# Kernel optimization log

Hardware: AMD Instinct MI355X
Metric: run time of the kernel (lower is better)

Reference implementation:

```python
import jax, jax.numpy as jnp
import numpy as np

T, D = 8192, 1024      # num flattened tokens, hidden_dim
E, K = 8, 2            # n_experts, num_experts_per_tok


def setup_inputs() -> dict:
    key = jax.random.key(0)
    k1, k2, k3, k4, k5 = jax.random.split(key, 5)
    x = jax.random.normal(k1, (T, D), dtype=jnp.float32)
    flat_expert_indices = jax.random.randint(k2, (T * K,), 0, E, dtype=jnp.int32)
    flat_expert_weights = jax.random.uniform(k3, (T * K,), dtype=jnp.float32)
    # Expert params: fc1/fc2 are bias-free Linears, stored torch-style [out, in]
    W1 = jax.random.normal(k4, (E, D, D), dtype=jnp.float32) * (1.0 / np.sqrt(D))
    W2 = jax.random.normal(k5, (E, D, D), dtype=jnp.float32) * (1.0 / np.sqrt(D))
    return {"x": x, "flat_expert_indices": flat_expert_indices,
            "flat_expert_weights": flat_expert_weights, "W1": W1, "W2": W2}


def reference(x, flat_expert_indices, flat_expert_weights, W1, W2):
    # DummyExpert: relu(relu(x @ W1.T) @ W2.T), per expert (torch Linear = x @ W.T)
    # Dense dispatch: compute every expert on every token, then gather the
    # top-k expert outputs per token and combine with routing weights.
    h = jax.nn.relu(jnp.einsum('td,eod->eto', x, W1))   # [E, T, D]
    y = jax.nn.relu(jnp.einsum('eto,epo->etp', h, W2))  # [E, T, D]
    idx = flat_expert_indices.reshape(T, K)             # [T, K]
    w = flat_expert_weights.reshape(T, K)               # [T, K]
    yt = jnp.transpose(y, (1, 0, 2))                    # [T, E, D]
    sel = jnp.take_along_axis(yt, idx[:, :, None].astype(jnp.int32), axis=1)  # [T, K, D]
    return jnp.sum(sel * w[:, :, None], axis=1)         # [T, D]
```

## Files before the change

kernel.cpp:

```cpp
#include <hip/hip_runtime.h>

typedef unsigned short u16;
typedef unsigned int   u32;
typedef unsigned long long u64;
typedef __attribute__((ext_vector_type(8))) short short8;
typedef __attribute__((ext_vector_type(4))) float f32x4;

#define T_TOK 8192
#define DIM   1024
#define NEXP  8
#define NPAIR (T_TOK * 2)
#define MAXTILES 136

__device__ __forceinline__ u16 f2bf(float f) {
  u32 u = __builtin_bit_cast(u32, f);
  u32 r = (u + 0x7fffu + ((u >> 16) & 1u)) >> 16;
  return (u16)r;
}
__device__ __forceinline__ float bf2f(u16 b) {
  return __builtin_bit_cast(float, ((u32)b) << 16);
}

__device__ __forceinline__ void gl_lds16(const u16* g, u16* l) {
  __builtin_amdgcn_global_load_lds(
      (const __attribute__((address_space(1))) u32*)g,
      (__attribute__((address_space(3))) u32*)l,
      16, 0, 0);
}

__global__ void prep_k(const float* __restrict__ x, const float* __restrict__ W1,
                       const float* __restrict__ W2,
                       u16* __restrict__ xb, u16* __restrict__ w1b, u16* __restrict__ w2b,
                       const int* __restrict__ idx,
                       int* __restrict__ counts, int* __restrict__ offsets,
                       int* __restrict__ bucket, int* __restrict__ pos,
                       int* __restrict__ tlist, int* __restrict__ ntiles) {
  __shared__ int lc[16][NEXP];
  __shared__ int lo[16][NEXP];

  if (blockIdx.x != 0) {
    const int g = ((int)(blockIdx.x - 1) * 1024 + (int)threadIdx.x) * 8;
    const int region = g >> 23;
    const int i = g & 0x7fffff;
    const float* s = (region == 0) ? x : (region == 1) ? W1 : W2;
    u16* d = (region == 0) ? xb : (region == 1) ? w1b : w2b;
    f32x4 a = *(const f32x4*)(s + i);
    f32x4 b = *(const f32x4*)(s + i + 4);
    short8 o;
    o[0] = (short)f2bf(a[0]); o[1] = (short)f2bf(a[1]);
    o[2] = (short)f2bf(a[2]); o[3] = (short)f2bf(a[3]);
    o[4] = (short)f2bf(b[0]); o[5] = (short)f2bf(b[1]);
    o[6] = (short)f2bf(b[2]); o[7] = (short)f2bf(b[3]);
    *(short8*)(d + i) = o;
    return;
  }

  const int tid  = threadIdx.x;
  const int w    = tid >> 6;
  const int lane = tid & 63;
  const u64 ltmask = (lane == 63) ? 0x7fffffffffffffffull : ((1ull << lane) - 1);

  int e_i[16];
#pragma unroll
  for (int i = 0; i < 16; ++i) e_i[i] = idx[(w * 16 + i) * 64 + lane];

  int cnt[NEXP] = {};
#pragma unroll
  for (int i = 0; i < 16; ++i) {
#pragma unroll
    for (int ex = 0; ex < NEXP; ++ex) {
      u64 m = __ballot(e_i[i] == ex);
      cnt[ex] += (int)__popcll(m);
    }
  }
  if (lane == 0) {
#pragma unroll
    for (int ex = 0; ex < NEXP; ++ex) lc[w][ex] = cnt[ex];
  }
  __syncthreads();

  if (tid == 0) {
    int s = 0;
    int c8[NEXP];
    for (int ex = 0; ex < NEXP; ++ex) {
      offsets[ex] = s;
      int c = 0;
      for (int ww = 0; ww < 16; ++ww) { lo[ww][ex] = s; s += lc[ww][ex]; c += lc[ww][ex]; }
      counts[ex] = c;
      c8[ex] = c;
    }
    int t = 0;
    for (int r = 0; r < 128; ++r)
      for (int ex = 0; ex < NEXP; ++ex)
        if (r * 128 < c8[ex]) tlist[t++] = (r << 3) | ex;
    *ntiles = t;
  }
  __syncthreads();

  int cur[NEXP];
#pragma unroll
  for (int ex = 0; ex < NEXP; ++ex) cur[ex] = lo[w][ex];
#pragma unroll
  for (int i = 0; i < 16; ++i) {
    const int item = (w * 16 + i) * 64 + lane;
    const int e = e_i[i];
    int p = 0;
#pragma unroll
    for (int ex = 0; ex < NEXP; ++ex) {
      u64 m = __ballot(e == ex);
      int rank = (int)__popcll(m & ltmask);
      if (e == ex) p = cur[ex] + rank;
      cur[ex] += (int)__popcll(m);
    }
    bucket[p] = item;
    pos[item] = p;
  }
}

template <int GATHER>
__global__ __launch_bounds__(256, 4)
void moe_gemm_k(const u16* __restrict__ A,
                const u16* __restrict__ W,
                u16* __restrict__ O,
                const int* __restrict__ counts,
                const int* __restrict__ offsets,
                const int* __restrict__ bucket,
                const int* __restrict__ tlist,
                const int* __restrict__ ntiles) {
  if ((int)blockIdx.x >= *ntiles) return;
  const int info = tlist[blockIdx.x];
  const int e    = info & 7;
  const int m0   = (info >> 3) << 7;
  const int cnt  = counts[e];
  const int seg  = offsets[e];
  const int n0   = blockIdx.y << 7;

  __shared__ u16 As[128 * 64];
  __shared__ u16 Bs[128 * 64];

  const int tid  = threadIdx.x;
  const int lane = tid & 63;
  const int wave = tid >> 6;

  int aoff[4], boff[4];
#pragma unroll
  for (int j = 0; j < 4; ++j) {
    const int c   = ((wave << 2) + j) * 64 + lane;
    const int r   = c >> 3;
    const int c16 = (c & 7) ^ (r & 7);
    int p = seg + m0 + r;
    p = (p < seg + cnt) ? p : (seg + cnt - 1);
    int rowbase;
    if (GATHER) { const int pair = bucket[p]; rowbase = (pair >> 1) * DIM; }
    else        { rowbase = p * DIM; }
    aoff[j] = rowbase + (c16 << 3);
    boff[j] = e * DIM * DIM + (n0 + r) * DIM + (c16 << 3);
  }

  f32x4 acc[4][4] = {};

  const int wm   = (wave >> 1) << 6;
  const int wn   = (wave & 1) << 6;
  const int lr   = lane & 15;
  const int quad = lane >> 4;

  for (int k0 = 0; k0 < DIM; k0 += 64) {
    __syncthreads();
#pragma unroll
    for (int j = 0; j < 4; ++j) {
      const int instr = (wave << 2) + j;
      gl_lds16(A + aoff[j] + k0, &As[instr << 9]);
      gl_lds16(W + boff[j] + k0, &Bs[instr << 9]);
    }
    __syncthreads();

#pragma unroll
    for (int kk = 0; kk < 64; kk += 32) {
      const int qb = (kk >> 3) + quad;
      short8 af[4], bf[4];
#pragma unroll
      for (int mi = 0; mi < 4; ++mi) {
        const int r = wm + (mi << 4) + lr;
        af[mi] = *(const short8*)&As[r * 64 + ((qb ^ (r & 7)) << 3)];
      }
#pragma unroll
      for (int ni = 0; ni < 4; ++ni) {
        const int r = wn + (ni << 4) + lr;
        bf[ni] = *(const short8*)&Bs[r * 64 + ((qb ^ (r & 7)) << 3)];
      }
#pragma unroll
      for (int mi = 0; mi < 4; ++mi)
#pragma unroll
        for (int ni = 0; ni < 4; ++ni)
          acc[mi][ni] = __builtin_amdgcn_mfma_f32_16x16x32_bf16(af[mi], bf[ni], acc[mi][ni], 0, 0, 0);
    }
  }

  const int pend = seg + cnt;
#pragma unroll
  for (int mi = 0; mi < 4; ++mi) {
#pragma unroll
    for (int ni = 0; ni < 4; ++ni) {
      const int col = n0 + wn + (ni << 4) + lr;
#pragma unroll
      for (int r4 = 0; r4 < 4; ++r4) {
        const int p = seg + m0 + wm + (mi << 4) + (quad << 2) + r4;
        if (p < pend) {
          float v = acc[mi][ni][r4];
          v = v > 0.f ? v : 0.f;
          O[(size_t)p * DIM + col] = f2bf(v);
        }
      }
    }
  }
}

__global__ void combine_k(const u16* __restrict__ y, const int* __restrict__ pos,
                          const float* __restrict__ wts, float* __restrict__ out) {
  const int t    = blockIdx.x * 2 + (threadIdx.x >> 7);
  const int lane = threadIdx.x & 127;
  const int col  = lane * 8;
  const int p0 = pos[2 * t], p1 = pos[2 * t + 1];
  const float w0 = wts[2 * t], w1 = wts[2 * t + 1];
  const short8 a = *(const short8*)(y + (size_t)p0 * DIM + col);
  const short8 b = *(const short8*)(y + (size_t)p1 * DIM + col);
  f32x4 o0, o1;
#pragma unroll
  for (int j = 0; j < 8; ++j) {
    float v = w0 * bf2f((u16)a[j]) + w1 * bf2f((u16)b[j]);
    if (j < 4) o0[j] = v; else o1[j - 4] = v;
  }
  float* op = out + (size_t)t * DIM + col;
  *(f32x4*)op = o0;
  *(f32x4*)(op + 4) = o1;
}

extern "C" void kernel_launch(void* const* d_in, const int* in_sizes, int n_in,
                              void* d_out, int out_size, void* d_ws, size_t ws_size,
                              hipStream_t stream) {
  const float* x   = (const float*)d_in[0];
  const int*   idx = (const int*)d_in[1];
  const float* wts = (const float*)d_in[2];
  const float* W1  = (const float*)d_in[3];
  const float* W2  = (const float*)d_in[4];
  float* out = (float*)d_out;

  char* ws = (char*)d_ws;
  int* counts  = (int*)ws;
  int* offsets = (int*)(ws + 32);
  int* ntiles  = (int*)(ws + 64);
  int* tlist   = (int*)(ws + 128);
  int* bucket  = (int*)(ws + 1024);
  int* pos     = (int*)(ws + 1024 + 4 * NPAIR);
  const size_t base = 132096;
  const size_t MB16 = 16ull * 1024 * 1024;
  u16* xb  = (u16*)(ws + base);
  u16* w1b = (u16*)(ws + base + MB16);
  u16* w2b = (u16*)(ws + base + 2 * MB16);
  u16* h   = (u16*)(ws + base + 3 * MB16);
  u16* yb  = xb;

  prep_k<<<3 * 1024 + 1, 1024, 0, stream>>>(x, W1, W2, xb, w1b, w2b,
                                            idx, counts, offsets, bucket, pos,
                                            tlist, ntiles);

  dim3 gg(MAXTILES, DIM / 128);
  moe_gemm_k<1><<<gg, 256, 0, stream>>>(xb, w1b, h, counts, offsets, bucket, tlist, ntiles);
  moe_gemm_k<0><<<gg, 256, 0, stream>>>(h, w2b, yb, counts, offsets, bucket, tlist, ntiles);

  combine_k<<<T_TOK / 2, 256, 0, stream>>>(yb, pos, wts, out);
}
```

Baseline: 244.7 us.

## Fuse weighted combine into second GEMM epilogue via float atomics

Removes the separate combine kernel and the intermediate bf16 expert-output buffer. The second GEMM now scales its ReLU output by the routing weight and atomically adds it into the fp32 output, which the prep kernel zeroes in extra blocks. This saves a kernel launch and a write-then-read of the intermediate, but adds scattered scalar fp32 atomics and makes the summation order nondeterministic.

```diff
diff --git a/kernel.cpp b/kernel.cpp
--- a/kernel.cpp
+++ b/kernel.cpp
@@ -17,9 +17,6 @@
   u32 r = (u + 0x7fffu + ((u >> 16) & 1u)) >> 16;
   return (u16)r;
 }
-__device__ __forceinline__ float bf2f(u16 b) {
-  return __builtin_bit_cast(float, ((u32)b) << 16);
-}
 
 __device__ __forceinline__ void gl_lds16(const u16* g, u16* l) {
   __builtin_amdgcn_global_load_lds(
@@ -31,27 +28,37 @@
 __global__ void prep_k(const float* __restrict__ x, const float* __restrict__ W1,
                        const float* __restrict__ W2,
                        u16* __restrict__ xb, u16* __restrict__ w1b, u16* __restrict__ w2b,
+                       float* __restrict__ out,
                        const int* __restrict__ idx,
                        int* __restrict__ counts, int* __restrict__ offsets,
-                       int* __restrict__ bucket, int* __restrict__ pos,
+                       int* __restrict__ bucket,
                        int* __restrict__ tlist, int* __restrict__ ntiles) {
   __shared__ int lc[16][NEXP];
   __shared__ int lo[16][NEXP];
 
-  if (blockIdx.x != 0) {
-    const int g = ((int)(blockIdx.x - 1) * 1024 + (int)threadIdx.x) * 8;
+  const int b = (int)blockIdx.x;
+  if (b >= 1 && b <= 3072) {
+    const int g = ((b - 1) * 1024 + (int)threadIdx.x) * 8;
     const int region = g >> 23;
     const int i = g & 0x7fffff;
     const float* s = (region == 0) ? x : (region == 1) ? W1 : W2;
     u16* d = (region == 0) ? xb : (region == 1) ? w1b : w2b;
     f32x4 a = *(const f32x4*)(s + i);
-    f32x4 b = *(const f32x4*)(s + i + 4);
+    f32x4 bb = *(const f32x4*)(s + i + 4);
     short8 o;
-    o[0] = (short)f2bf(a[0]); o[1] = (short)f2bf(a[1]);
-    o[2] = (short)f2bf(a[2]); o[3] = (short)f2bf(a[3]);
-    o[4] = (short)f2bf(b[0]); o[5] = (short)f2bf(b[1]);
-    o[6] = (short)f2bf(b[2]); o[7] = (short)f2bf(b[3]);
+    o[0] = (short)f2bf(a[0]);  o[1] = (short)f2bf(a[1]);
+    o[2] = (short)f2bf(a[2]);  o[3] = (short)f2bf(a[3]);
+    o[4] = (short)f2bf(bb[0]); o[5] = (short)f2bf(bb[1]);
+    o[6] = (short)f2bf(bb[2]); o[7] = (short)f2bf(bb[3]);
     *(short8*)(d + i) = o;
+    return;
+  }
+  if (b > 3072) {
+    float* o0 = out + (size_t)(b - 3073) * 65536;
+    const f32x4 zero = {0.f, 0.f, 0.f, 0.f};
+#pragma unroll
+    for (int ii = 0; ii < 16; ++ii)
+      *(f32x4*)(o0 + ii * 4096 + threadIdx.x * 4) = zero;
     return;
   }
 
@@ -113,15 +120,16 @@
       cur[ex] += (int)__popcll(m);
     }
     bucket[p] = item;
-    pos[item] = p;
-  }
-}
-
-template <int GATHER>
+  }
+}
+
+template <int MODE>
 __global__ __launch_bounds__(256, 4)
 void moe_gemm_k(const u16* __restrict__ A,
                 const u16* __restrict__ W,
                 u16* __restrict__ O,
+                float* __restrict__ out,
+                const float* __restrict__ wts,
                 const int* __restrict__ counts,
                 const int* __restrict__ offsets,
                 const int* __restrict__ bucket,
@@ -151,8 +159,8 @@
     int p = seg + m0 + r;
     p = (p < seg + cnt) ? p : (seg + cnt - 1);
     int rowbase;
-    if (GATHER) { const int pair = bucket[p]; rowbase = (pair >> 1) * DIM; }
-    else        { rowbase = p * DIM; }
+    if (MODE == 0) { const int pair = bucket[p]; rowbase = (pair >> 1) * DIM; }
+    else           { rowbase = p * DIM; }
     aoff[j] = rowbase + (c16 << 3);
     boff[j] = e * DIM * DIM + (n0 + r) * DIM + (c16 << 3);
   }
@@ -199,40 +207,45 @@
   const int pend = seg + cnt;
 #pragma unroll
   for (int mi = 0; mi < 4; ++mi) {
-#pragma unroll
-    for (int ni = 0; ni < 4; ++ni) {
-      const int col = n0 + wn + (ni << 4) + lr;
+    if (MODE == 0) {
+#pragma unroll
+      for (int ni = 0; ni < 4; ++ni) {
+        const int col = n0 + wn + (ni << 4) + lr;
+#pragma unroll
+        for (int r4 = 0; r4 < 4; ++r4) {
+          const int p = seg + m0 + wm + (mi << 4) + (quad << 2) + r4;
+          if (p < pend) {
+            float v = acc[mi][ni][r4];
+            v = v > 0.f ? v : 0.f;
+            O[(size_t)p * DIM + col] = f2bf(v);
+          }
+        }
+      }
+    } else {
+      bool ok[4]; float wr[4]; int tr[4];
 #pragma unroll
       for (int r4 = 0; r4 < 4; ++r4) {
         const int p = seg + m0 + wm + (mi << 4) + (quad << 2) + r4;
-        if (p < pend) {
-          float v = acc[mi][ni][r4];
-          v = v > 0.f ? v : 0.f;
-          O[(size_t)p * DIM + col] = f2bf(v);
+        ok[r4] = (p < pend);
+        const int pair = ok[r4] ? bucket[p] : 0;
+        wr[r4] = ok[r4] ? wts[pair] : 0.f;
+        tr[r4] = pair >> 1;
+      }
+#pragma unroll
+      for (int ni = 0; ni < 4; ++ni) {
+        const int col = n0 + wn + (ni << 4) + lr;
+#pragma unroll
+        for (int r4 = 0; r4 < 4; ++r4) {
+          if (ok[r4]) {
+            float v = acc[mi][ni][r4];
+            v = v > 0.f ? v : 0.f;
+            __hip_atomic_fetch_add(out + (size_t)tr[r4] * DIM + col, wr[r4] * v,
+                                   __ATOMIC_RELAXED, __HIP_MEMORY_SCOPE_AGENT);
+          }
         }
       }
     }
   }
-}
-
-__global__ void combine_k(const u16* __restrict__ y, const int* __restrict__ pos,
-                          const float* __restrict__ wts, float* __restrict__ out) {
-  const int t    = blockIdx.x * 2 + (threadIdx.x >> 7);
-  const int lane = threadIdx.x & 127;
-  const int col  = lane * 8;
-  const int p0 = pos[2 * t], p1 = pos[2 * t + 1];
-  const float w0 = wts[2 * t], w1 = wts[2 * t + 1];
-  const short8 a = *(const short8*)(y + (size_t)p0 * DIM + col);
-  const short8 b = *(const short8*)(y + (size_t)p1 * DIM + col);
-  f32x4 o0, o1;
-#pragma unroll
-  for (int j = 0; j < 8; ++j) {
-    float v = w0 * bf2f((u16)a[j]) + w1 * bf2f((u16)b[j]);
-    if (j < 4) o0[j] = v; else o1[j - 4] = v;
-  }
-  float* op = out + (size_t)t * DIM + col;
-  *(f32x4*)op = o0;
-  *(f32x4*)(op + 4) = o1;
 }
 
 extern "C" void kernel_launch(void* const* d_in, const int* in_sizes, int n_in,
@@ -251,22 +264,19 @@
   int* ntiles  = (int*)(ws + 64);
   int* tlist   = (int*)(ws + 128);
   int* bucket  = (int*)(ws + 1024);
-  int* pos     = (int*)(ws + 1024 + 4 * NPAIR);
   const size_t base = 132096;
   const size_t MB16 = 16ull * 1024 * 1024;
   u16* xb  = (u16*)(ws + base);
   u16* w1b = (u16*)(ws + base + MB16);
   u16* w2b = (u16*)(ws + base + 2 * MB16);
   u16* h   = (u16*)(ws + base + 3 * MB16);
-  u16* yb  = xb;
-
-  prep_k<<<3 * 1024 + 1, 1024, 0, stream>>>(x, W1, W2, xb, w1b, w2b,
-                                            idx, counts, offsets, bucket, pos,
-                                            tlist, ntiles);
+
+  prep_k<<<3201, 1024, 0, stream>>>(x, W1, W2, xb, w1b, w2b, out,
+                                    idx, counts, offsets, bucket, tlist, ntiles);
 
   dim3 gg(MAXTILES, DIM / 128);
-  moe_gemm_k<1><<<gg, 256, 0, stream>>>(xb, w1b, h, counts, offsets, bucket, tlist, ntiles);
-  moe_gemm_k<0><<<gg, 256, 0, stream>>>(h, w2b, yb, counts, offsets, bucket, tlist, ntiles);
-
-  combine_k<<<T_TOK / 2, 256, 0, stream>>>(yb, pos, wts, out);
-}
+  moe_gemm_k<0><<<gg, 256, 0, stream>>>(xb, w1b, h, nullptr, nullptr,
+                                        counts, offsets, bucket, tlist, ntiles);
+  moe_gemm_k<1><<<gg, 256, 0, stream>>>(h, w2b, nullptr, out, wts,
+                                        counts, offsets, bucket, tlist, ntiles);
+}
```

Result: slower. 280.9 us (+14.8%).

## Double-buffer LDS tiles with BK=32 to overlap global loads and MFMA

Applied to the files above, without the earlier changes.

Replaces the single 128x64 LDS tile per operand with two 128x32 ping-pong buffers. The global-to-LDS loads for the next K slice are issued before computing on the current one, so memory latency is hidden behind MFMA work. The swizzled layout is reworked so two rows pack into each 64-element LDS line, and one barrier is removed per step. In exchange, K steps are smaller, giving twice as many barriers per unit of work, and correctness depends on the new swizzle indexing.

```diff
diff --git a/kernel.cpp b/kernel.cpp
--- a/kernel.cpp
+++ b/kernel.cpp
@@ -135,26 +135,30 @@
   const int seg  = offsets[e];
   const int n0   = blockIdx.y << 7;
 
-  __shared__ u16 As[128 * 64];
-  __shared__ u16 Bs[128 * 64];
+  __shared__ u16 As0[4096];
+  __shared__ u16 As1[4096];
+  __shared__ u16 Bs0[4096];
+  __shared__ u16 Bs1[4096];
 
   const int tid  = threadIdx.x;
   const int lane = tid & 63;
   const int wave = tid >> 6;
 
-  int aoff[4], boff[4];
-#pragma unroll
-  for (int j = 0; j < 4; ++j) {
-    const int c   = ((wave << 2) + j) * 64 + lane;
-    const int r   = c >> 3;
-    const int c16 = (c & 7) ^ (r & 7);
+  int aoff[2], boff[2];
+#pragma unroll
+  for (int j = 0; j < 2; ++j) {
+    const int c  = ((wave << 1) + j) * 64 + lane;
+    const int R  = c >> 3;
+    const int pp = (c & 7) ^ (R & 7);
+    const int q  = pp & 3;
+    const int r  = (R << 1) + (pp >> 2);
     int p = seg + m0 + r;
     p = (p < seg + cnt) ? p : (seg + cnt - 1);
     int rowbase;
     if (GATHER) { const int pair = bucket[p]; rowbase = (pair >> 1) * DIM; }
     else        { rowbase = p * DIM; }
-    aoff[j] = rowbase + (c16 << 3);
-    boff[j] = e * DIM * DIM + (n0 + r) * DIM + (c16 << 3);
+    aoff[j] = rowbase + (q << 3);
+    boff[j] = e * DIM * DIM + (n0 + r) * DIM + (q << 3);
   }
 
   f32x4 acc[4][4] = {};
@@ -164,37 +168,62 @@
   const int lr   = lane & 15;
   const int quad = lane >> 4;
 
-  for (int k0 = 0; k0 < DIM; k0 += 64) {
+  int ard[4], brd[4];
+#pragma unroll
+  for (int mi = 0; mi < 4; ++mi) {
+    const int r = wm + (mi << 4) + lr;
+    const int R = r >> 1;
+    ard[mi] = (R << 6) + (((((r & 1) << 2) + quad) ^ (R & 7)) << 3);
+  }
+#pragma unroll
+  for (int ni = 0; ni < 4; ++ni) {
+    const int r = wn + (ni << 4) + lr;
+    const int R = r >> 1;
+    brd[ni] = (R << 6) + (((((r & 1) << 2) + quad) ^ (R & 7)) << 3);
+  }
+
+#define STAGE_K(k0, Adst, Bdst)                                          \
+  {                                                                      \
+    _Pragma("unroll")                                                    \
+    for (int j = 0; j < 2; ++j) {                                        \
+      const int instr = (wave << 1) + j;                                 \
+      gl_lds16(A + aoff[j] + (k0), &Adst[instr << 9]);                   \
+      gl_lds16(W + boff[j] + (k0), &Bdst[instr << 9]);                   \
+    }                                                                    \
+  }
+
+#define COMPUTE_K(Asrc, Bsrc)                                            \
+  {                                                                      \
+    short8 af[4], bf[4];                                                 \
+    _Pragma("unroll")                                                    \
+    for (int mi = 0; mi < 4; ++mi) af[mi] = *(const short8*)&Asrc[ard[mi]]; \
+    _Pragma("unroll")                                                    \
+    for (int ni = 0; ni < 4; ++ni) bf[ni] = *(const short8*)&Bsrc[brd[ni]]; \
+    _Pragma("unroll")                                                    \
+    for (int mi = 0; mi < 4; ++mi)                                       \
+      _Pragma("unroll")                                                  \
+      for (int ni = 0; ni < 4; ++ni)                                     \
+        acc[mi][ni] = __builtin_amdgcn_mfma_f32_16x16x32_bf16(           \
+            af[mi], bf[ni], acc[mi][ni], 0, 0, 0);                       \
+  }
+
+  STAGE_K(0, As0, Bs0);
+  __syncthreads();
+
+  for (int t = 0; t < DIM / 32; t += 2) {
+    STAGE_K((t + 1) << 5, As1, Bs1);
+    COMPUTE_K(As0, Bs0);
     __syncthreads();
-#pragma unroll
-    for (int j = 0; j < 4; ++j) {
-      const int instr = (wave << 2) + j;
-      gl_lds16(A + aoff[j] + k0, &As[instr << 9]);
-      gl_lds16(W + boff[j] + k0, &Bs[instr << 9]);
-    }
-    __syncthreads();
-
-#pragma unroll
-    for (int kk = 0; kk < 64; kk += 32) {
-      const int qb = (kk >> 3) + quad;
-      short8 af[4], bf[4];
-#pragma unroll
-      for (int mi = 0; mi < 4; ++mi) {
-        const int r = wm + (mi << 4) + lr;
-        af[mi] = *(const short8*)&As[r * 64 + ((qb ^ (r & 7)) << 3)];
-      }
-#pragma unroll
-      for (int ni = 0; ni < 4; ++ni) {
-        const int r = wn + (ni << 4) + lr;
-        bf[ni] = *(const short8*)&Bs[r * 64 + ((qb ^ (r & 7)) << 3)];
-      }
-#pragma unroll
-      for (int mi = 0; mi < 4; ++mi)
-#pragma unroll
-        for (int ni = 0; ni < 4; ++ni)
-          acc[mi][ni] = __builtin_amdgcn_mfma_f32_16x16x32_bf16(af[mi], bf[ni], acc[mi][ni], 0, 0, 0);
-    }
-  }
+    if (t + 2 < DIM / 32) {
+      STAGE_K((t + 2) << 5, As0, Bs0);
+      COMPUTE_K(As1, Bs1);
+      __syncthreads();
+    } else {
+      COMPUTE_K(As1, Bs1);
+    }
+  }
+#undef STAGE_K
+#undef COMPUTE_K
 
   const int pend = seg + cnt;
 #pragma unroll
```

Result: slower. 558.6 us (+128.3%).
